# Optimization experiments

Measured on AMD Instinct MI355X. Metric: run time of the kernel, lower is better.

The kernel has to match this reference:

```python
import jax, jax.numpy as jnp
import numpy as np

WS = 8        # window_size
NH = 16       # num_heads
EPS = 1e-5    # BatchNorm eps (inference mode: running_mean=0, running_var=1)

def conv2d(x, w, padding=0, groups=1):
    return jax.lax.conv_general_dilated(
        x, w, (1, 1), [(padding, padding), (padding, padding)],
        dimension_numbers=('NCHW', 'OIHW', 'NCHW'), feature_group_count=groups)

def bn(x, gamma, beta):
    # eval-mode BatchNorm with running_mean=0, running_var=1
    return x * (gamma / jnp.sqrt(1.0 + EPS))[None, :, None, None] + beta[None, :, None, None]

def avgpool(x, kh, kw, ph, pw):
    # torch AvgPool2d with count_include_pad=True: sum over zero-padded window / (kh*kw)
    s = jax.lax.reduce_window(x, 0.0, jax.lax.add, (1, 1, kh, kw), (1, 1, 1, 1),
                              [(0, 0), (0, 0), (ph, ph), (pw, pw)])
    return s / float(kh * kw)

def rel_pos_index(ws):
    coords = np.stack(np.meshgrid(np.arange(ws), np.arange(ws), indexing='ij')).reshape(2, -1)
    rel = (coords[:, :, None] - coords[:, None, :]).transpose(1, 2, 0) + (ws - 1)
    return (rel[..., 0] * (2 * ws - 1) + rel[..., 1]).reshape(-1)

def hge_kernels(W):
    # build 4 directional Sobel kernels + Gaussian-Laplacian from learned scalars
    S0, S45, S90 = W[:, :, 0, 0], W[:, :, 0, 1], W[:, :, 0, 2]
    S135, GL = W[:, :, 1, 0], W[:, :, 2, 2]
    z = jnp.zeros_like(S0)
    k3 = lambda rows: jnp.stack([jnp.stack(r, -1) for r in rows], -2)  # [O,I,3,3]
    w0 = k3([[S0, 2*S0, S0], [z, z, z], [-S0, -2*S0, -S0]])
    w45 = k3([[2*S45, S45, z], [S45, z, -S45], [z, -S45, -2*S45]])
    w90 = k3([[S90, z, -S90], [2*S90, z, -2*S90], [S90, z, -S90]])
    w135 = k3([[z, -S135, -2*S135], [S135, z, -S135], [2*S135, S135, z]])
    a1 = GL * 4.0; a2 = -a1 / 8.0; a3 = -a1 / 16.0
    wGL = jnp.zeros(S0.shape + (5, 5), S0.dtype)
    for i, j, v in [(0,2,a3),(1,1,a3),(1,2,a2),(1,3,a3),(2,0,a3),(2,1,a2),(2,2,a1),
                    (2,3,a2),(2,4,a3),(3,1,a3),(3,2,a2),(3,3,a3),(4,2,a3)]:
        wGL = wGL.at[:, :, i, j].set(v)
    return w0, w45, w90, w135, wGL

def forward(x, ca_h1, ca_w1, ca_fh, ca_fw, l1_w, l1_g, l1_b, l2_w, l2_g, l2_b,
            hge_w, hge_fc_w, hge_fc_b, qkv_w, rel_table, proj_dw, proj_g, proj_b, proj_pw):
    B, C, H, W = x.shape
    d = C // NH
    scale = d ** -0.5
    # --- CA block: coordinate attention (1x1 convs on H- and W-pooled features) ---
    cm = lambda w, t: jnp.einsum('oc,bc...->bo...', w, t)
    s_h = jax.nn.sigmoid(cm(ca_fh, cm(ca_h1, x.mean(3))))   # [B,C,H]
    s_w = jax.nn.sigmoid(cm(ca_fw, cm(ca_w1, x.mean(2))))   # [B,C,W]
    x = x * s_h[:, :, :, None] * s_w[:, :, None, :]
    # --- local branch: 1x1 ConvBN + 3x3 ConvBN + HGE edge operator ---
    local = bn(conv2d(x, l2_w), l2_g, l2_b) + bn(conv2d(x, l1_w, padding=1), l1_g, l1_b)
    w0, w45, w90, w135, wGL = hge_kernels(hge_w)
    feats = jnp.concatenate([conv2d(x, w0, 1), conv2d(x, w45, 1), conv2d(x, w90, 1),
                             conv2d(x, w135, 1), conv2d(x, wGL, 2)], axis=1)  # [B,5C,H,W]
    local = local + conv2d(feats, hge_fc_w) + hge_fc_b[None, :, None, None]
    # --- windowed attention ---
    ph, pw = (-H) % WS, (-W) % WS
    if ph or pw:
        x = jnp.pad(x, ((0, 0), (0, 0), (0, ph), (0, pw)), mode='reflect')
    Hp, Wp = x.shape[2], x.shape[3]
    hh, ww = Hp // WS, Wp // WS
    qkv = conv2d(x, qkv_w)                                   # [B,3C,Hp,Wp]
    qkv = qkv.reshape(B, 3, NH, d, hh, WS, ww, WS)
    qkv = qkv.transpose(1, 0, 4, 6, 2, 5, 7, 3).reshape(3, B * hh * ww, NH, WS * WS, d)
    q, k, v = qkv[0], qkv[1], qkv[2]
    bias = rel_table[rel_pos_index(WS)].reshape(WS * WS, WS * WS, NH).transpose(2, 0, 1)
    dots = jnp.einsum('wnid,wnjd->wnij', q, k) * scale + bias[None]
    attn = jax.nn.softmax(dots, axis=-1)
    o = jnp.einsum('wnij,wnjd->wnid', attn, v)
    o = o.reshape(B, hh, ww, NH, WS, WS, d).transpose(0, 3, 6, 1, 4, 2, 5)
    o = o.reshape(B, C, Hp, Wp)[:, :, :H, :W]
    # --- directional average pooling of attention output ---
    ox = avgpool(jnp.pad(o, ((0, 0), (0, 0), (0, 1), (0, 0)), mode='reflect'), WS, 1, WS // 2 - 1, 0)
    oy = avgpool(jnp.pad(o, ((0, 0), (0, 0), (0, 0), (0, 1)), mode='reflect'), 1, WS, 0, WS // 2 - 1)
    out = ox + oy + local
    # --- pad_out + separable ConvBN projection (depthwise k=ws -> BN -> 1x1) ---
    out = jnp.pad(out, ((0, 0), (0, 0), (0, 1), (0, 1)), mode='reflect')
    out = conv2d(out, proj_dw, padding=(WS - 1) // 2, groups=C)
    out = bn(out, proj_g, proj_b)
    out = conv2d(out, proj_pw)
    return out[:, :, :H, :W]

def setup_inputs() -> dict:
    key = jax.random.key(0)
    ks = jax.random.split(key, 20)
    C = 128
    f32 = jnp.float32
    n = lambda k, sh, s: jax.random.normal(k, sh, f32) * s
    return {
        'x': jax.random.normal(ks[0], (2, C, 256, 256), f32),
        'ca_h1': n(ks[1], (C, C), 0.05), 'ca_w1': n(ks[2], (C, C), 0.05),
        'ca_fh': n(ks[3], (C, C), 0.05), 'ca_fw': n(ks[4], (C, C), 0.05),
        'l1_w': n(ks[5], (C, C, 3, 3), 0.03),
        'l1_g': 1.0 + n(ks[6], (C,), 0.02), 'l1_b': n(ks[7], (C,), 0.02),
        'l2_w': n(ks[8], (C, C, 1, 1), 0.09),
        'l2_g': 1.0 + n(ks[9], (C,), 0.02), 'l2_b': n(ks[10], (C,), 0.02),
        'hge_w': n(ks[11], (C, C, 3, 3), 0.02),
        'hge_fc_w': n(ks[12], (C, 5 * C, 1, 1), 0.02), 'hge_fc_b': n(ks[13], (C,), 0.02),
        'qkv_w': n(ks[14], (3 * C, C, 1, 1), 0.05),
        'rel_table': n(ks[15], ((2 * WS - 1) ** 2, NH), 0.02),
        'proj_dw': n(ks[16], (C, 1, WS, WS), 0.05),
        'proj_g': 1.0 + n(ks[17], (C,), 0.02), 'proj_b': n(ks[18], (C,), 0.02),
        'proj_pw': n(ks[19], (C, C, 1, 1), 0.05),
    }

def reference(x, ca_h1, ca_w1, ca_fh, ca_fw, l1_w, l1_g, l1_b, l2_w, l2_g, l2_b,
              hge_w, hge_fc_w, hge_fc_b, qkv_w, rel_table, proj_dw, proj_g, proj_b, proj_pw):
    return forward(x, ca_h1, ca_w1, ca_fh, ca_fw, l1_w, l1_g, l1_b, l2_w, l2_g, l2_b,
                   hge_w, hge_fc_w, hge_fc_b, qkv_w, rel_table, proj_dw, proj_g, proj_b, proj_pw)
```

## Files before the change

kernel.cpp:

```cpp
#include <hip/hip_runtime.h>

#define BB 2
#define CC 128
#define HWSZ 65536
#define RSQE 0.9999950000374997f
#define ATT_SCALE 0.35355339059327373f

typedef unsigned short u16;
using short8 = __attribute__((ext_vector_type(8))) short;
using f32x4  = __attribute__((ext_vector_type(4))) float;

#if defined(__has_builtin)
# if __has_builtin(__builtin_amdgcn_fdot2_f32_bf16)
#  define HAVE_DOT2 1
# endif
#endif

__device__ __forceinline__ float b2f(u16 u){
  return __uint_as_float(((unsigned int)u) << 16);
}
__device__ __forceinline__ u16 f2b(float f){
  unsigned int v = __float_as_uint(f);
  unsigned int r = (v + 0x7FFFu + ((v >> 16) & 1u)) >> 16;
  return (u16)r;
}

__device__ const int c_DI[13] = {-2,-1,-1,-1, 0, 0,0,0,0, 1,1,1, 2};
__device__ const int c_DJ[13] = { 0,-1, 0, 1,-2,-1,0,1,2,-1,0,1, 0};

__global__ void k_detect(const u16* __restrict__ xr, int* __restrict__ flag){
  __shared__ int ws_[4];
  int tid = threadIdx.x;
  int cnt = 0;
  for (int i = 0; i < 16; ++i){
    u16 u = xr[tid*16 + i];
    int e = (u >> 7) & 0xFF;
    cnt += (e < 100 || e > 141) ? 1 : 0;
  }
  #pragma unroll
  for (int off = 32; off > 0; off >>= 1) cnt += __shfl_down(cnt, off, 64);
  if ((tid & 63) == 0) ws_[tid >> 6] = cnt;
  __syncthreads();
  if (tid == 0) *flag = (ws_[0]+ws_[1]+ws_[2]+ws_[3] > 64) ? 1 : 0;
}

__global__ void k_ingest4(const void* __restrict__ src, u16* __restrict__ dst,
                          int n4, const int* __restrict__ flag){
  int i = blockIdx.x * 256 + threadIdx.x;
  if (i >= n4) return;
  if (*flag){
    float4 f = ((const float4*)src)[i];
    ushort4 r; r.x=f2b(f.x); r.y=f2b(f.y); r.z=f2b(f.z); r.w=f2b(f.w);
    ((ushort4*)dst)[i] = r;
  } else {
    ((ushort4*)dst)[i] = ((const ushort4*)src)[i];
  }
}

struct PtrL { const void* p[19]; };

__global__ void k_ingest_w(PtrL pl, u16* __restrict__ dst, const int* __restrict__ flag){
  const int ends[19] = {16384,32768,49152,65536,212992,213120,213248,229632,229760,
                        229888,377344,459264,459392,508544,512144,520336,520464,520592,536976};
  int g = blockIdx.x * 256 + threadIdx.x;
  int idx = g * 4;
  if (idx >= 536976) return;
  int seg = 0, start = 0;
  #pragma unroll
  for (int s = 0; s < 19; ++s){ if (idx >= ends[s]){ seg = s+1; start = ends[s]; } }
  int local = idx - start;
  const void* sp = pl.p[seg];
  if (*flag){
    float4 f = ((const float4*)sp)[local >> 2];
    ushort4 r; r.x=f2b(f.x); r.y=f2b(f.y); r.z=f2b(f.z); r.w=f2b(f.w);
    *(ushort4*)(dst + idx) = r;
  } else {
    *(ushort4*)(dst + idx) = ((const ushort4*)sp)[local >> 2];
  }
}

__global__ void k_prep_A(const u16* __restrict__ fh, const u16* __restrict__ h1,
                         const u16* __restrict__ fw, const u16* __restrict__ w1,
                         const u16* __restrict__ l1b, const u16* __restrict__ l2b,
                         const u16* __restrict__ fcb,
                         float* __restrict__ A_h, float* __restrict__ A_w,
                         float* __restrict__ biasK){
  int idx = blockIdx.x * 256 + threadIdx.x;
  int o = idx >> 7, c = idx & 127;
  float ah = 0.f, aw = 0.f;
  for (int m = 0; m < 128; ++m){
    ah += b2f(fh[o*128 + m]) * b2f(h1[m*128 + c]);
    aw += b2f(fw[o*128 + m]) * b2f(w1[m*128 + c]);
  }
  A_h[idx] = ah; A_w[idx] = aw;
  if (c == 0) biasK[o] = b2f(l1b[o]) + b2f(l2b[o]) + b2f(fcb[o]);
}

__global__ void k_prep_K(const u16* __restrict__ hge_w, const u16* __restrict__ fc_w,
                         const u16* __restrict__ l1_w, const u16* __restrict__ l1_g,
                         const u16* __restrict__ l2_w, const u16* __restrict__ l2_g,
                         u16* __restrict__ Kwb){
  int idx = blockIdx.x * 256 + threadIdx.x;
  int o = idx >> 7, c = idx & 127;
  float m0=0.f, m45=0.f, m90=0.f, m135=0.f, mgl=0.f;
  const u16* fo = fc_w + o*640;
  for (int m = 0; m < 128; ++m){
    const u16* hw9 = hge_w + (size_t)(m*128 + c)*9;
    m0   += b2f(fo[m      ]) * b2f(hw9[0]);
    m45  += b2f(fo[128 + m]) * b2f(hw9[1]);
    m90  += b2f(fo[256 + m]) * b2f(hw9[2]);
    m135 += b2f(fo[384 + m]) * b2f(hw9[3]);
    mgl  += b2f(fo[512 + m]) * b2f(hw9[8]);
  }
  float g1 = b2f(l1_g[o]) * RSQE;
  float g2 = b2f(l2_g[o]) * RSQE;
  float l1v[9];
  #pragma unroll
  for (int t = 0; t < 9; ++t) l1v[t] = b2f(l1_w[(size_t)idx*9 + t]) * g1;
  float l2v = b2f(l2_w[idx]) * g2;
  float kp[13];
  kp[0]  = -0.25f*mgl;
  kp[1]  =  m0 + 2.f*m45 + m90              - 0.25f*mgl + l1v[0];
  kp[2]  =  2.f*m0 + m45 - m135             - 0.50f*mgl + l1v[1];
  kp[3]  =  m0 - m90 - 2.f*m135             - 0.25f*mgl + l1v[2];
  kp[4]  = -0.25f*mgl;
  kp[5]  =  m45 + 2.f*m90 + m135            - 0.50f*mgl + l1v[3];
  kp[6]  =  4.f*mgl + l1v[4] + l2v;
  kp[7]  = -m45 - 2.f*m90 - m135            - 0.50f*mgl + l1v[5];
  kp[8]  = -0.25f*mgl;
  kp[9]  = -m0 + m90 + 2.f*m135             - 0.25f*mgl + l1v[6];
  kp[10] = -2.f*m0 - m45 + m135             - 0.50f*mgl + l1v[7];
  kp[11] = -m0 - 2.f*m45 - m90              - 0.25f*mgl + l1v[8];
  kp[12] = -0.25f*mgl;
  #pragma unroll
  for (int t = 0; t < 13; ++t) Kwb[t*16384 + idx] = f2b(kp[t]);
}

__global__ void k_means(const u16* __restrict__ x, float* __restrict__ mh, float* __restrict__ mw){
  __shared__ float colpart[4][256];
  int c = blockIdx.x, b = blockIdx.y;
  const u16* xp = x + (size_t)(b*CC + c)*HWSZ;
  int tid = threadIdx.x, lane = tid & 63, wv = tid >> 6;
  float c0=0.f,c1=0.f,c2=0.f,c3=0.f;
  for (int r = 0; r < 64; ++r){
    int h = wv*64 + r;
    ushort4 u = *(const ushort4*)(xp + h*256 + lane*4);
    float v0=b2f(u.x), v1=b2f(u.y), v2=b2f(u.z), v3=b2f(u.w);
    c0+=v0; c1+=v1; c2+=v2; c3+=v3;
    float rs = v0+v1+v2+v3;
    #pragma unroll
    for (int off = 32; off > 0; off >>= 1) rs += __shfl_down(rs, off, 64);
    if (lane == 0) mh[(size_t)(b*CC + c)*256 + h] = rs * (1.0f/256.0f);
  }
  colpart[wv][lane*4+0]=c0; colpart[wv][lane*4+1]=c1;
  colpart[wv][lane*4+2]=c2; colpart[wv][lane*4+3]=c3;
  __syncthreads();
  mw[(size_t)(b*CC + c)*256 + tid] =
    (colpart[0][tid]+colpart[1][tid]+colpart[2][tid]+colpart[3][tid]) * (1.0f/256.0f);
}

__global__ void k_sig(const float* __restrict__ A_h, const float* __restrict__ A_w,
                      const float* __restrict__ mh, const float* __restrict__ mw,
                      float* __restrict__ s_h, float* __restrict__ s_w){
  int o = blockIdx.x, b = blockIdx.y, sel = blockIdx.z, t = threadIdx.x;
  const float* A = sel ? A_w : A_h;
  const float* m = sel ? mw : mh;
  float* s = sel ? s_w : s_h;
  float acc = 0.f;
  for (int c = 0; c < 128; ++c)
    acc += A[o*128 + c] * m[(size_t)(b*CC + c)*256 + t];
  s[(size_t)(b*CC + o)*256 + t] = 1.0f / (1.0f + __expf(-acc));
}

__global__ void k_scale2cl(const u16* __restrict__ cx, const float* __restrict__ s_h,
                           const float* __restrict__ s_w, u16* __restrict__ xcl){
  __shared__ u16 t[16][136];
  int b = blockIdx.z >> 8, h = blockIdx.z & 255;
  int w0 = blockIdx.x * 16;
  int tid = threadIdx.x;
  int ic = tid >> 1, wseg = (tid & 1) * 8;
  uint4 v = *(const uint4*)(cx + (size_t)(b*CC + ic)*HWSZ + h*256 + w0 + wseg);
  float sh = s_h[(size_t)(b*CC + ic)*256 + h];
  const float* swp = s_w + (size_t)(b*CC + ic)*256 + w0 + wseg;
  float4 swa = *(const float4*)swp;
  float4 swb = *(const float4*)(swp + 4);
  u16 tmp[8]; *(uint4*)tmp = v;
  t[wseg+0][ic] = f2b(b2f(tmp[0])*sh*swa.x);
  t[wseg+1][ic] = f2b(b2f(tmp[1])*sh*swa.y);
  t[wseg+2][ic] = f2b(b2f(tmp[2])*sh*swa.z);
  t[wseg+3][ic] = f2b(b2f(tmp[3])*sh*swa.w);
  t[wseg+4][ic] = f2b(b2f(tmp[4])*sh*swb.x);
  t[wseg+5][ic] = f2b(b2f(tmp[5])*sh*swb.y);
  t[wseg+6][ic] = f2b(b2f(tmp[6])*sh*swb.z);
  t[wseg+7][ic] = f2b(b2f(tmp[7])*sh*swb.w);
  __syncthreads();
  int w = tid >> 4, part = (tid & 15) * 8;
  uint4 o = *(const uint4*)&t[w][part];
  *(uint4*)(xcl + ((size_t)(b*256 + h)*256 + (w0 + w))*128 + part) = o;
}

__global__ void k_cf2cl(const u16* __restrict__ src, u16* __restrict__ dst){
  __shared__ u16 t[16][136];
  int b = blockIdx.z >> 8, h = blockIdx.z & 255;
  int w0 = blockIdx.x * 16;
  int tid = threadIdx.x;
  int ic = tid >> 1, wseg = (tid & 1) * 8;
  uint4 v = *(const uint4*)(src + (size_t)(b*CC + ic)*HWSZ + h*256 + w0 + wseg);
  u16 tmp[8]; *(uint4*)tmp = v;
  #pragma unroll
  for (int k = 0; k < 8; ++k) t[wseg + k][ic] = tmp[k];
  __syncthreads();
  int w = tid >> 4, part = (tid & 15) * 8;
  uint4 o = *(const uint4*)&t[w][part];
  *(uint4*)(dst + ((size_t)(b*256 + h)*256 + (w0 + w))*128 + part) = o;
}

__launch_bounds__(256)
__global__ void k_conv5m(const u16* __restrict__ xcl, const u16* __restrict__ Kwb,
                         const float* __restrict__ biasK, u16* __restrict__ outp){
  __shared__ u16 As[128][40];
  __shared__ u16 Bs[128][40];
  int tid = threadIdx.x;
  int wv = tid >> 6, lane = tid & 63;
  int q = lane >> 4, l16 = lane & 15;
  int pt = blockIdx.x;
  int b = pt >> 9, h = (pt >> 1) & 255, w0 = (pt & 1) << 7;
  int mrow = (wv & 1) << 6, nrow = (wv >> 1) << 6;
  int sr = tid >> 2, sp = (tid & 3) << 3;
  const u16* xb_b = xcl + (size_t)b*HWSZ*128;
  f32x4 acc[4][4];
  #pragma unroll
  for (int mt = 0; mt < 4; ++mt)
    #pragma unroll
    for (int nt = 0; nt < 4; ++nt) acc[mt][nt] = (f32x4){0.f,0.f,0.f,0.f};

  for (int kc = 0; kc < 52; ++kc){
    int t = kc >> 2, c0 = (kc & 3) << 5;
    int di = c_DI[t], dj = c_DJ[t];
    int hh2 = h + di;
    bool rowok = (unsigned)hh2 < 256u;
    const u16* rowp = xb_b + (size_t)(rowok ? hh2 : 0)*256*128 + c0 + sp;
    int col0 = w0 + dj + sr;
    int col1 = col0 + 64;
    __syncthreads();
    {
      uint4 va0 = {0,0,0,0}, va1 = {0,0,0,0};
      if (rowok && (unsigned)col0 < 256u) va0 = *(const uint4*)(rowp + col0*128);
      if (rowok && (unsigned)col1 < 256u) va1 = *(const uint4*)(rowp + col1*128);
      *(uint4*)&As[sr][sp] = va0;
      *(uint4*)&As[sr + 64][sp] = va1;
      const u16* Bb = Kwb + t*16384 + c0;
      *(uint4*)&Bs[sr][sp] = *(const uint4*)(Bb + sr*128 + sp);
      *(uint4*)&Bs[sr + 64][sp] = *(const uint4*)(Bb + (sr + 64)*128 + sp);
    }
    __syncthreads();
    short8 af[4], bf[4];
    #pragma unroll
    for (int mt = 0; mt < 4; ++mt) af[mt] = *(const short8*)&As[mrow + mt*16 + l16][q*8];
    #pragma unroll
    for (int nt = 0; nt < 4; ++nt) bf[nt] = *(const short8*)&Bs[nrow + nt*16 + l16][q*8];
    #pragma unroll
    for (int mt = 0; mt < 4; ++mt)
      #pragma unroll
      for (int nt = 0; nt < 4; ++nt)
        acc[mt][nt] = __builtin_amdgcn_mfma_f32_16x16x32_bf16(af[mt], bf[nt], acc[mt][nt], 0, 0, 0);
  }
  #pragma unroll
  for (int nt = 0; nt < 4; ++nt){
    int n = nrow + nt*16 + l16;
    float bv = biasK[n];
    size_t cbase = (size_t)(b*CC + n)*HWSZ + h*256 + w0;
    #pragma unroll
    for (int mt = 0; mt < 4; ++mt){
      int m = mrow + mt*16 + q*4;
      ushort4 st;
      st.x = f2b(acc[mt][nt][0] + bv);
      st.y = f2b(acc[mt][nt][1] + bv);
      st.z = f2b(acc[mt][nt][2] + bv);
      st.w = f2b(acc[mt][nt][3] + bv);
      *(ushort4*)(outp + cbase + m) = st;
    }
  }
}

__launch_bounds__(256)
__global__ void k_mgemm(const u16* __restrict__ Xcl, const u16* __restrict__ W,
                        u16* __restrict__ Y, float* __restrict__ Yf,
                        const int* __restrict__ flag, int nsel, int mode){
  __shared__ u16 As[128][136];
  __shared__ u16 Bs[128][136];
  int tid = threadIdx.x;
  int wv = tid >> 6, lane = tid & 63;
  int q = lane >> 4, l16 = lane & 15;
  int pt = blockIdx.x;
  int b = pt >> 9, h = (pt >> 1) & 255, w0 = (pt & 1) << 7;
  int mrow = (wv & 1) << 6, nrow = (wv >> 1) << 6;
  const u16* Abase = Xcl + ((size_t)(b*256 + h)*256 + w0)*128;
  #pragma unroll
  for (int i = 0; i < 8; ++i){
    int seg = i*256 + tid;
    *(uint4*)&As[seg >> 4][(seg & 15) << 3] = *(const uint4*)(Abase + seg*8);
  }
  for (int sel = 0; sel < nsel; ++sel){
    __syncthreads();
    const u16* Wb = W + sel*16384;
    #pragma unroll
    for (int i = 0; i < 8; ++i){
      int seg = i*256 + tid;
      *(uint4*)&Bs[seg >> 4][(seg & 15) << 3] = *(const uint4*)(Wb + seg*8);
    }
    __syncthreads();
    f32x4 acc[4][4];
    #pragma unroll
    for (int mt = 0; mt < 4; ++mt)
      #pragma unroll
      for (int nt = 0; nt < 4; ++nt) acc[mt][nt] = (f32x4){0.f,0.f,0.f,0.f};
    #pragma unroll
    for (int kc = 0; kc < 4; ++kc){
      short8 af[4], bf[4];
      #pragma unroll
      for (int mt = 0; mt < 4; ++mt) af[mt] = *(const short8*)&As[mrow + mt*16 + l16][kc*32 + q*8];
      #pragma unroll
      for (int nt = 0; nt < 4; ++nt) bf[nt] = *(const short8*)&Bs[nrow + nt*16 + l16][kc*32 + q*8];
      #pragma unroll
      for (int mt = 0; mt < 4; ++mt)
        #pragma unroll
        for (int nt = 0; nt < 4; ++nt)
          acc[mt][nt] = __builtin_amdgcn_mfma_f32_16x16x32_bf16(af[mt], bf[nt], acc[mt][nt], 0, 0, 0);
    }
    if (mode == 0){
      __syncthreads();
      #pragma unroll
      for (int mt = 0; mt < 4; ++mt){
        int m0i = mrow + mt*16 + q*4;
        #pragma unroll
        for (int nt = 0; nt < 4; ++nt){
          int n = nrow + nt*16 + l16;
          Bs[m0i+0][n] = f2b(acc[mt][nt][0]);
          Bs[m0i+1][n] = f2b(acc[mt][nt][1]);
          Bs[m0i+2][n] = f2b(acc[mt][nt][2]);
          Bs[m0i+3][n] = f2b(acc[mt][nt][3]);
        }
      }
      __syncthreads();
      int win = tid >> 4, head = tid & 15;
      size_t obase = (((((size_t)b*32 + (h >> 3))*32 + (w0 >> 3) + win)*3 + sel)*16 + head)*512
                     + (size_t)(h & 7)*64;
      #pragma unroll
      for (int pj = 0; pj < 8; ++pj){
        uint4 vv = *(const uint4*)&Bs[win*8 + pj][head*8];
        *(uint4*)(Y + obase + pj*8) = vv;
      }
    } else {
      int f32o = (Yf != nullptr) && (*flag != 0);
      #pragma unroll
      for (int nt = 0; nt < 4; ++nt){
        int n = nrow + nt*16 + l16;
        size_t cbase = (size_t)(b*CC + n)*HWSZ + h*256 + w0;
        #pragma unroll
        for (int mt = 0; mt < 4; ++mt){
          int m = mrow + mt*16 + q*4;
          if (f32o){
            float4 st; st.x=acc[mt][nt][0]; st.y=acc[mt][nt][1];
            st.z=acc[mt][nt][2]; st.w=acc[mt][nt][3];
            *(float4*)(Yf + cbase + m) = st;
          } else {
            ushort4 st;
            st.x = f2b(acc[mt][nt][0]); st.y = f2b(acc[mt][nt][1]);
            st.z = f2b(acc[mt][nt][2]); st.w = f2b(acc[mt][nt][3]);
            *(ushort4*)(Y + cbase + m) = st;
          }
        }
      }
    }
  }
}

__launch_bounds__(128)
__global__ void k_attn2(const u16* __restrict__ qkvw, const u16* __restrict__ rel,
                        u16* __restrict__ obuf){
  __shared__ float relf[16*228];
  __shared__ u16  qls[2][64][8];
  __shared__ u16  kls[2][64][8];
  __shared__ float vls[2][64][8];
  __shared__ u16  ols[2][64][8];
  int tid = threadIdx.x, wv = tid >> 6, lane = tid & 63;
  int b = blockIdx.z, hh = blockIdx.y, ww0 = blockIdx.x * 2;
  for (int e = tid; e < 3600; e += 128){
    int hd = e / 225, i = e - hd*225;
    relf[hd*228 + i] = b2f(rel[i*16 + hd]);
  }
  int qi = lane >> 3, qj = lane & 7;
  const float* rbase0 = relf + ((qi + 7)*15 + (qj + 7) - 112);
  size_t blkbase = (((size_t)b*32 + hh)*32 + ww0)*3*8192;
  __syncthreads();

  for (int head = 0; head < 16; ++head){
    __syncthreads();
    #pragma unroll
    for (int s = 0; s < 2; ++s){
      int seg = s*128 + tid;
      int sel = seg >> 7, win = (seg >> 6) & 1, pos = seg & 63;
      uint4 v = *(const uint4*)(qkvw + blkbase + (size_t)win*24576 + sel*8192 + head*512 + pos*8);
      if (sel == 0) *(uint4*)&qls[win][pos][0] = v;
      else          *(uint4*)&kls[win][pos][0] = v;
    }
    {
      int win = tid >> 6, pos = tid & 63;
      uint4 raw = *(const uint4*)(qkvw + blkbase + (size_t)win*24576 + 2*8192 + head*512 + pos*8);
      u16 tv[8]; *(uint4*)tv = raw;
      float4 lo, hi;
      lo.x=b2f(tv[0]); lo.y=b2f(tv[1]); lo.z=b2f(tv[2]); lo.w=b2f(tv[3]);
      hi.x=b2f(tv[4]); hi.y=b2f(tv[5]); hi.z=b2f(tv[6]); hi.w=b2f(tv[7]);
      *(float4*)&vls[win][pos][0] = lo;
      *(float4*)&vls[win][pos][4] = hi;
    }
    __syncthreads();

    uint4 qv = *(const uint4*)&qls[wv][lane][0];
    const float* rp = rbase0 + head*228;
    float s[64];
#if HAVE_DOT2
    typedef __bf16 bf2 __attribute__((ext_vector_type(2)));
    bf2 q0 = __builtin_bit_cast(bf2, qv.x), q1 = __builtin_bit_cast(bf2, qv.y);
    bf2 q2 = __builtin_bit_cast(bf2, qv.z), q3 = __builtin_bit_cast(bf2, qv.w);
    #pragma unroll
    for (int kp = 0; kp < 64; ++kp){
      uint4 kv = *(const uint4*)&kls[wv][kp][0];
      float d = __builtin_amdgcn_fdot2_f32_bf16(q3, __builtin_bit_cast(bf2, kv.w), 0.f, false);
      d = __builtin_amdgcn_fdot2_f32_bf16(q2, __builtin_bit_cast(bf2, kv.z), d, false);
      d = __builtin_amdgcn_fdot2_f32_bf16(q1, __builtin_bit_cast(bf2, kv.y), d, false);
      d = __builtin_amdgcn_fdot2_f32_bf16(q0, __builtin_bit_cast(bf2, kv.x), d, false);
      s[kp] = fmaf(d, ATT_SCALE, rp[112 - (kp>>3)*15 - (kp&7)]);
    }
#else
    float qf[8];
    { u16 tq[8]; *(uint4*)tq = qv;
      #pragma unroll
      for (int d = 0; d < 8; ++d) qf[d] = b2f(tq[d]); }
    #pragma unroll
    for (int kp = 0; kp < 64; ++kp){
      uint4 kv = *(const uint4*)&kls[wv][kp][0];
      u16 tk[8]; *(uint4*)tk = kv;
      float d = 0.f;
      #pragma unroll
      for (int dd = 0; dd < 8; ++dd) d = fmaf(qf[dd], b2f(tk[dd]), d);
      s[kp] = fmaf(d, ATT_SCALE, rp[112 - (kp>>3)*15 - (kp&7)]);
    }
#endif
    float t16[16];
    #pragma unroll
    for (int i = 0; i < 16; ++i)
      t16[i] = fmaxf(fmaxf(s[i], s[i+16]), fmaxf(s[i+32], s[i+48]));
    float mx = t16[0];
    #pragma unroll
    for (int i = 1; i < 16; ++i) mx = fmaxf(mx, t16[i]);
    #pragma unroll
    for (int kp = 0; kp < 64; ++kp) s[kp] = __expf(s[kp] - mx);
    #pragma unroll
    for (int i = 0; i < 16; ++i)
      t16[i] = (s[i] + s[i+16]) + (s[i+32] + s[i+48]);
    float sum = t16[0];
    #pragma unroll
    for (int i = 1; i < 16; ++i) sum += t16[i];
    float inv = 1.0f / sum;
    float ov[8] = {0.f,0.f,0.f,0.f,0.f,0.f,0.f,0.f};
    #pragma unroll
    for (int kp = 0; kp < 64; ++kp){
      float4 va = *(const float4*)&vls[wv][kp][0];
      float4 vb = *(const float4*)&vls[wv][kp][4];
      float pp = s[kp];
      ov[0] = fmaf(pp, va.x, ov[0]); ov[1] = fmaf(pp, va.y, ov[1]);
      ov[2] = fmaf(pp, va.z, ov[2]); ov[3] = fmaf(pp, va.w, ov[3]);
      ov[4] = fmaf(pp, vb.x, ov[4]); ov[5] = fmaf(pp, vb.y, ov[5]);
      ov[6] = fmaf(pp, vb.z, ov[6]); ov[7] = fmaf(pp, vb.w, ov[7]);
    }
    u16 po[8];
    #pragma unroll
    for (int d = 0; d < 8; ++d) po[d] = f2b(ov[d] * inv);
    *(uint4*)&ols[wv][lane][0] = *(uint4*)po;
    __syncthreads();
    {
      int win = tid >> 6, d = (tid >> 3) & 7, r = tid & 7;
      u16 pk[8];
      #pragma unroll
      for (int wl = 0; wl < 8; ++wl) pk[wl] = ols[win][r*8 + wl][d];
      *(uint4*)(obuf + (size_t)(b*CC + head*8 + d)*HWSZ + (hh*8 + r)*256 + (ww0 + win)*8)
        = *(uint4*)pk;
    }
  }
}

__launch_bounds__(256)
__global__ void k_pool2(const u16* __restrict__ obuf, u16* __restrict__ localb){
  __shared__ u16 t[71][88];
  int bc = blockIdx.z;
  int h0 = blockIdx.y * 64, w0 = blockIdx.x * 64;
  int tid = threadIdx.x;
  const u16* op = obuf + (size_t)bc * HWSZ;

  for (int e = tid; e < 710; e += 256){
    int tr = e / 10, ci = e - tr*10;
    int gt = h0 - 3 + tr;
    if (gt == 256) gt = 254;
    bool rv = (unsigned)gt <= 255u;
    int g0 = w0 - 8 + ci*8;
    uint4 v = {0,0,0,0};
    if (rv){
      if (g0 >= 0 && g0 <= 248){
        v = *(const uint4*)(op + gt*256 + g0);
      } else {
        u16 tmp[8];
        #pragma unroll
        for (int j = 0; j < 8; ++j){
          int g = g0 + j;
          if (g == 256) g = 254;
          tmp[j] = ((unsigned)g <= 255u) ? op[gt*256 + g] : (u16)0;
        }
        v = *(const uint4*)tmp;
      }
    }
    *(uint4*)&t[tr][ci*8] = v;
  }
  __syncthreads();

  int ty = tid >> 4, tx = tid & 15;
  int r0 = ty*4, c0 = tx*4;
  float sxv[4][4];
  #pragma unroll
  for (int c = 0; c < 4; ++c){
    float col[11];
    #pragma unroll
    for (int i = 0; i < 11; ++i) col[i] = b2f(t[r0+i][c0+8+c]);
    float s = ((col[0]+col[1])+(col[2]+col[3]))+((col[4]+col[5])+(col[6]+col[7]));
    sxv[0][c] = s;
    s += col[8]  - col[0]; sxv[1][c] = s;
    s += col[9]  - col[1]; sxv[2][c] = s;
    s += col[10] - col[2]; sxv[3][c] = s;
  }
  #pragma unroll
  for (int r = 0; r < 4; ++r){
    int rr = r0 + r;
    float pre[11];
    #pragma unroll
    for (int j = 0; j < 11; ++j) pre[j] = b2f(t[rr+3][c0+5+j]);
    float sy0 = ((pre[0]+pre[1])+(pre[2]+pre[3]))+((pre[4]+pre[5])+(pre[6]+pre[7]));
    float sy1 = sy0 + pre[8]  - pre[0];
    float sy2 = sy1 + pre[9]  - pre[1];
    float sy3 = sy2 + pre[10] - pre[2];
    size_t base = (size_t)bc*HWSZ + (size_t)(h0+rr)*256 + (w0+c0);
    ushort4 lv = *(const ushort4*)(localb + base);
    ushort4 st;
    st.x = f2b((sxv[r][0]+sy0)*0.125f + b2f(lv.x));
    st.y = f2b((sxv[r][1]+sy1)*0.125f + b2f(lv.y));
    st.z = f2b((sxv[r][2]+sy2)*0.125f + b2f(lv.z));
    st.w = f2b((sxv[r][3]+sy3)*0.125f + b2f(lv.w));
    *(ushort4*)(localb + base) = st;
  }
}

__launch_bounds__(256)
__global__ void k_dw2(const u16* __restrict__ u_, const u16* __restrict__ dww,
                      const u16* __restrict__ g, const u16* __restrict__ bta,
                      u16* __restrict__ dwout){
  __shared__ u16 xt[71][152];
  int c = blockIdx.z & 127, b = blockIdx.z >> 7;
  int h0 = blockIdx.y * 64, w0 = blockIdx.x * 128;
  int tid = threadIdx.x;
  const u16* up = u_ + (size_t)(b*CC + c)*HWSZ;

  for (int e = tid; e < 71*18; e += 256){
    int tr = e / 18, ci = e - tr*18;
    int gt = h0 - 3 + tr;
    if (gt == 256) gt = 254;
    int g0 = w0 - 8 + ci*8;
    uint4 v = {0,0,0,0};
    if ((unsigned)gt <= 255u){
      if (g0 >= 0 && g0 <= 248){
        v = *(const uint4*)(up + gt*256 + g0);
      } else {
        u16 tmp[8];
        #pragma unroll
        for (int j = 0; j < 8; ++j){
          int gw = g0 + j;
          if (gw == 256) gw = 254;
          tmp[j] = ((unsigned)gw <= 255u) ? up[gt*256 + gw] : (u16)0;
        }
        v = *(const uint4*)tmp;
      }
    }
    *(uint4*)&xt[tr][ci*8] = v;
  }

#if HAVE_DOT2
  typedef __bf16 bf2v __attribute__((ext_vector_type(2)));
  unsigned int wp[32];
  {
    const uint4* wsrc = (const uint4*)(dww + c*64);
    #pragma unroll
    for (int t = 0; t < 8; ++t){
      uint4 v = wsrc[t];
      wp[t*4+0]=v.x; wp[t*4+1]=v.y; wp[t*4+2]=v.z; wp[t*4+3]=v.w;
    }
  }
#else
  float wf[64];
  {
    const u16* wsrc = dww + c*64;
    #pragma unroll
    for (int t = 0; t < 64; ++t) wf[t] = b2f(wsrc[t]);
  }
#endif
  __syncthreads();

  int tx = tid & 15, ty = tid >> 4;
  int r0 = ty*4;
  int cb = tx*8;
  float acc[4][8];
  #pragma unroll
  for (int r = 0; r < 4; ++r)
    #pragma unroll
    for (int k = 0; k < 8; ++k) acc[r][k] = 0.f;

  #pragma unroll
  for (int i = 0; i < 11; ++i){
    const u16* rowp = &xt[r0 + i][cb + 4];
    uint2 av = *(const uint2*)(rowp);
    uint4 mv = *(const uint4*)(rowp + 4);
    uint2 zv = *(const uint2*)(rowp + 12);
    unsigned int d0=av.x, d1=av.y, d2=mv.x, d3=mv.y, d4=mv.z, d5=mv.w, d6=zv.x, d7=zv.y;
    unsigned int dd[8] = {d0,d1,d2,d3,d4,d5,d6,d7};
#if HAVE_DOT2
    unsigned int xp[15];
    #pragma unroll
    for (int t = 1; t < 15; ++t)
      xp[t] = (t & 1) ? ((dd[t>>1] >> 16) | (dd[(t>>1)+1] << 16)) : dd[t>>1];
    #pragma unroll
    for (int dr = 0; dr < 4; ++dr){
      int wr = i - dr;
      if (wr >= 0 && wr < 8){
        #pragma unroll
        for (int k = 0; k < 8; ++k){
          float s = acc[dr][k];
          #pragma unroll
          for (int p = 0; p < 4; ++p)
            s = __builtin_amdgcn_fdot2_f32_bf16(
                  __builtin_bit_cast(bf2v, wp[wr*4+p]),
                  __builtin_bit_cast(bf2v, xp[1+k+2*p]), s, false);
          acc[dr][k] = s;
        }
      }
    }
#else
    float xw[16];
    #pragma unroll
    for (int t = 1; t < 16; ++t){
      unsigned int w32 = dd[t>>1];
      xw[t] = __uint_as_float((t & 1) ? (w32 & 0xFFFF0000u) : (w32 << 16));
    }
    #pragma unroll
    for (int dr = 0; dr < 4; ++dr){
      int wr = i - dr;
      if (wr >= 0 && wr < 8){
        #pragma unroll
        for (int k = 0; k < 8; ++k){
          float s = acc[dr][k];
          #pragma unroll
          for (int j = 0; j < 8; ++j)
            s = fmaf(wf[wr*8+j], xw[1+k+j], s);
          acc[dr][k] = s;
        }
      }
    }
#endif
  }

  float scale = b2f(g[c]) * RSQE;
  float bb = b2f(bta[c]);
  size_t obase = (size_t)(b*CC + c)*HWSZ + (size_t)(h0 + r0)*256 + w0 + cb;
  #pragma unroll
  for (int r = 0; r < 4; ++r){
    u16 po[8];
    #pragma unroll
    for (int k = 0; k < 8; ++k) po[k] = f2b(acc[r][k]*scale + bb);
    *(uint4*)(dwout + obase + (size_t)r*256) = *(uint4*)po;
  }
}

extern "C" void kernel_launch(void* const* d_in, const int* in_sizes, int n_in,
                              void* d_out, int out_size, void* d_ws, size_t ws_size,
                              hipStream_t stream) {
  char* p = (char*)d_ws;
  u16* cx     = (u16*)p; p += 33554432;
  u16* xcl    = (u16*)p; p += 33554432;
  u16* qkvb   = (u16*)p; p += 100663296;
  u16* cw     = (u16*)p; p += 1074176;
  float* A_h    = (float*)p; p += 65536;
  float* A_w    = (float*)p; p += 65536;
  u16*  Kwb     = (u16*)p;  p += 425984;
  float* biasK  = (float*)p; p += 1024;
  float* mh     = (float*)p; p += 262144;
  float* mw     = (float*)p; p += 262144;
  float* s_h    = (float*)p; p += 262144;
  float* s_w    = (float*)p; p += 262144;
  int* flag     = (int*)p;   p += 256;

  u16* localb = (u16*)d_out;
  u16* qkvw   = qkvb;
  u16* obuf   = cx;
  u16* dwbuf  = qkvb;
  u16* dwcl   = xcl;

  const int O_h1=0, O_w1=16384, O_fh=32768, O_fw=49152, O_l1w=65536, O_l1g=212992,
            O_l1b=213120, O_l2w=213248, O_l2g=229632, O_l2b=229760, O_hge=229888,
            O_fcw=377344, O_fcb=459264, O_qkvw=459392, O_rel=508544, O_dw=512144,
            O_pg=520336, O_pb=520464, O_pw=520592;

  k_detect<<<1, 256, 0, stream>>>((const u16*)d_in[0], flag);
  k_ingest4<<<16384, 256, 0, stream>>>(d_in[0], cx, 4194304, flag);
  PtrL pl;
  for (int i = 0; i < 19; ++i) pl.p[i] = d_in[i+1];
  k_ingest_w<<<525, 256, 0, stream>>>(pl, cw, flag);

  k_prep_A<<<64, 256, 0, stream>>>(cw+O_fh, cw+O_h1, cw+O_fw, cw+O_w1,
                                   cw+O_l1b, cw+O_l2b, cw+O_fcb, A_h, A_w, biasK);
  k_prep_K<<<64, 256, 0, stream>>>(cw+O_hge, cw+O_fcw, cw+O_l1w, cw+O_l1g,
                                   cw+O_l2w, cw+O_l2g, Kwb);
  k_means<<<dim3(128, 2), 256, 0, stream>>>(cx, mh, mw);
  k_sig<<<dim3(128, 2, 2), 256, 0, stream>>>(A_h, A_w, mh, mw, s_h, s_w);
  k_scale2cl<<<dim3(16, 1, 512), 256, 0, stream>>>(cx, s_h, s_w, xcl);

  k_conv5m<<<1024, 256, 0, stream>>>(xcl, Kwb, biasK, localb);
  k_mgemm<<<1024, 256, 0, stream>>>(xcl, cw+O_qkvw, qkvw, nullptr, flag, 3, 0);
  k_attn2<<<dim3(16, 32, 2), 128, 0, stream>>>(qkvw, cw+O_rel, obuf);
  k_pool2<<<dim3(4, 4, 256), 256, 0, stream>>>(obuf, localb);
  k_dw2<<<dim3(2, 4, 256), 256, 0, stream>>>(localb, cw+O_dw, cw+O_pg, cw+O_pb, dwbuf);
  k_cf2cl<<<dim3(16, 1, 512), 256, 0, stream>>>(dwbuf, dwcl);
  k_mgemm<<<1024, 256, 0, stream>>>(dwcl, cw+O_pw, (u16*)d_out, (float*)d_out, flag, 1, 1);
}
```

Before: 606.9 us.

## Parallelize window attention across heads with one window per wave

The attention kernel is restructured so each block handles one head for four windows, one window per wave, instead of looping over all 16 heads for two windows. The relative-position table is converted to float once by a new small prep kernel rather than per block. The output is now written directly from registers as scattered 2-byte stores, with no LDS transpose and no per-head syncthreads. This gives far more blocks and fewer barriers, at the cost of less coalesced output writes.

Result: faster. 572.0 us (-5.8%).

```diff
diff --git a/kernel.cpp b/kernel.cpp
--- a/kernel.cpp
+++ b/kernel.cpp
@@ -94,6 +94,13 @@
   }
   A_h[idx] = ah; A_w[idx] = aw;
   if (c == 0) biasK[o] = b2f(l1b[o]) + b2f(l2b[o]) + b2f(fcb[o]);
+}
+
+__global__ void k_prep_rel(const u16* __restrict__ rel, float* __restrict__ relo){
+  int idx = blockIdx.x * 256 + threadIdx.x;
+  if (idx >= 3600) return;
+  int head = idx / 225, i = idx - head*225;
+  relo[idx] = b2f(rel[i*16 + head]);
 }
 
 __global__ void k_prep_K(const u16* __restrict__ hge_w, const u16* __restrict__ fc_w,
@@ -376,119 +383,94 @@
   }
 }
 
-__launch_bounds__(128)
-__global__ void k_attn2(const u16* __restrict__ qkvw, const u16* __restrict__ rel,
+__launch_bounds__(256)
+__global__ void k_attn3(const u16* __restrict__ qkvw, const float* __restrict__ relo,
                         u16* __restrict__ obuf){
-  __shared__ float relf[16*228];
-  __shared__ u16  qls[2][64][8];
-  __shared__ u16  kls[2][64][8];
-  __shared__ float vls[2][64][8];
-  __shared__ u16  ols[2][64][8];
+  __shared__ float relf[228];
+  __shared__ u16  kls[4][64][8];
+  __shared__ float vls[4][64][8];
   int tid = threadIdx.x, wv = tid >> 6, lane = tid & 63;
-  int b = blockIdx.z, hh = blockIdx.y, ww0 = blockIdx.x * 2;
-  for (int e = tid; e < 3600; e += 128){
-    int hd = e / 225, i = e - hd*225;
-    relf[hd*228 + i] = b2f(rel[i*16 + hd]);
-  }
+  int b = blockIdx.z >> 4, head = blockIdx.z & 15;
+  int hh = blockIdx.y, ww = blockIdx.x * 4 + wv;
+
+  for (int e = tid; e < 225; e += 256) relf[e] = relo[head*225 + e];
+
+  size_t base = (((size_t)b*32 + hh)*32 + ww)*3*8192 + (size_t)head*512;
+  uint4 qv = *(const uint4*)(qkvw + base + lane*8);
+  *(uint4*)&kls[wv][lane][0] = *(const uint4*)(qkvw + base + 8192 + lane*8);
+  {
+    uint4 raw = *(const uint4*)(qkvw + base + 16384 + lane*8);
+    u16 tv[8]; *(uint4*)tv = raw;
+    float4 lo, hi;
+    lo.x=b2f(tv[0]); lo.y=b2f(tv[1]); lo.z=b2f(tv[2]); lo.w=b2f(tv[3]);
+    hi.x=b2f(tv[4]); hi.y=b2f(tv[5]); hi.z=b2f(tv[6]); hi.w=b2f(tv[7]);
+    *(float4*)&vls[wv][lane][0] = lo;
+    *(float4*)&vls[wv][lane][4] = hi;
+  }
+  __syncthreads();
+
   int qi = lane >> 3, qj = lane & 7;
-  const float* rbase0 = relf + ((qi + 7)*15 + (qj + 7) - 112);
-  size_t blkbase = (((size_t)b*32 + hh)*32 + ww0)*3*8192;
-  __syncthreads();
-
-  for (int head = 0; head < 16; ++head){
-    __syncthreads();
-    #pragma unroll
-    for (int s = 0; s < 2; ++s){
-      int seg = s*128 + tid;
-      int sel = seg >> 7, win = (seg >> 6) & 1, pos = seg & 63;
-      uint4 v = *(const uint4*)(qkvw + blkbase + (size_t)win*24576 + sel*8192 + head*512 + pos*8);
-      if (sel == 0) *(uint4*)&qls[win][pos][0] = v;
-      else          *(uint4*)&kls[win][pos][0] = v;
-    }
-    {
-      int win = tid >> 6, pos = tid & 63;
-      uint4 raw = *(const uint4*)(qkvw + blkbase + (size_t)win*24576 + 2*8192 + head*512 + pos*8);
-      u16 tv[8]; *(uint4*)tv = raw;
-      float4 lo, hi;
-      lo.x=b2f(tv[0]); lo.y=b2f(tv[1]); lo.z=b2f(tv[2]); lo.w=b2f(tv[3]);
-      hi.x=b2f(tv[4]); hi.y=b2f(tv[5]); hi.z=b2f(tv[6]); hi.w=b2f(tv[7]);
-      *(float4*)&vls[win][pos][0] = lo;
-      *(float4*)&vls[win][pos][4] = hi;
-    }
-    __syncthreads();
-
-    uint4 qv = *(const uint4*)&qls[wv][lane][0];
-    const float* rp = rbase0 + head*228;
-    float s[64];
+  const float* rbase = relf + (qi + 7)*15 + (qj + 7);
+  float s[64];
 #if HAVE_DOT2
-    typedef __bf16 bf2 __attribute__((ext_vector_type(2)));
-    bf2 q0 = __builtin_bit_cast(bf2, qv.x), q1 = __builtin_bit_cast(bf2, qv.y);
-    bf2 q2 = __builtin_bit_cast(bf2, qv.z), q3 = __builtin_bit_cast(bf2, qv.w);
-    #pragma unroll
-    for (int kp = 0; kp < 64; ++kp){
-      uint4 kv = *(const uint4*)&kls[wv][kp][0];
-      float d = __builtin_amdgcn_fdot2_f32_bf16(q3, __builtin_bit_cast(bf2, kv.w), 0.f, false);
-      d = __builtin_amdgcn_fdot2_f32_bf16(q2, __builtin_bit_cast(bf2, kv.z), d, false);
-      d = __builtin_amdgcn_fdot2_f32_bf16(q1, __builtin_bit_cast(bf2, kv.y), d, false);
-      d = __builtin_amdgcn_fdot2_f32_bf16(q0, __builtin_bit_cast(bf2, kv.x), d, false);
-      s[kp] = fmaf(d, ATT_SCALE, rp[112 - (kp>>3)*15 - (kp&7)]);
-    }
+  typedef __bf16 bf2 __attribute__((ext_vector_type(2)));
+  bf2 q0 = __builtin_bit_cast(bf2, qv.x), q1 = __builtin_bit_cast(bf2, qv.y);
+  bf2 q2 = __builtin_bit_cast(bf2, qv.z), q3 = __builtin_bit_cast(bf2, qv.w);
+  #pragma unroll
+  for (int kp = 0; kp < 64; ++kp){
+    uint4 kv = *(const uint4*)&kls[wv][kp][0];
+    float d = __builtin_amdgcn_fdot2_f32_bf16(q3, __builtin_bit_cast(bf2, kv.w), 0.f, false);
+    d = __builtin_amdgcn_fdot2_f32_bf16(q2, __builtin_bit_cast(bf2, kv.z), d, false);
+    d = __builtin_amdgcn_fdot2_f32_bf16(q1, __builtin_bit_cast(bf2, kv.y), d, false);
+    d = __builtin_amdgcn_fdot2_f32_bf16(q0, __builtin_bit_cast(bf2, kv.x), d, false);
+    s[kp] = fmaf(d, ATT_SCALE, rbase[-((kp>>3)*15 + (kp&7))]);
+  }
 #else
-    float qf[8];
-    { u16 tq[8]; *(uint4*)tq = qv;
-      #pragma unroll
-      for (int d = 0; d < 8; ++d) qf[d] = b2f(tq[d]); }
-    #pragma unroll
-    for (int kp = 0; kp < 64; ++kp){
-      uint4 kv = *(const uint4*)&kls[wv][kp][0];
-      u16 tk[8]; *(uint4*)tk = kv;
-      float d = 0.f;
-      #pragma unroll
-      for (int dd = 0; dd < 8; ++dd) d = fmaf(qf[dd], b2f(tk[dd]), d);
-      s[kp] = fmaf(d, ATT_SCALE, rp[112 - (kp>>3)*15 - (kp&7)]);
-    }
+  float qf[8];
+  { u16 tq[8]; *(uint4*)tq = qv;
+    #pragma unroll
+    for (int d = 0; d < 8; ++d) qf[d] = b2f(tq[d]); }
+  #pragma unroll
+  for (int kp = 0; kp < 64; ++kp){
+    uint4 kv = *(const uint4*)&kls[wv][kp][0];
+    u16 tk[8]; *(uint4*)tk = kv;
+    float d = 0.f;
+    #pragma unroll
+    for (int dd = 0; dd < 8; ++dd) d = fmaf(qf[dd], b2f(tk[dd]), d);
+    s[kp] = fmaf(d, ATT_SCALE, rbase[-((kp>>3)*15 + (kp&7))]);
+  }
 #endif
-    float t16[16];
-    #pragma unroll
-    for (int i = 0; i < 16; ++i)
-      t16[i] = fmaxf(fmaxf(s[i], s[i+16]), fmaxf(s[i+32], s[i+48]));
-    float mx = t16[0];
-    #pragma unroll
-    for (int i = 1; i < 16; ++i) mx = fmaxf(mx, t16[i]);
-    #pragma unroll
-    for (int kp = 0; kp < 64; ++kp) s[kp] = __expf(s[kp] - mx);
-    #pragma unroll
-    for (int i = 0; i < 16; ++i)
-      t16[i] = (s[i] + s[i+16]) + (s[i+32] + s[i+48]);
-    float sum = t16[0];
-    #pragma unroll
-    for (int i = 1; i < 16; ++i) sum += t16[i];
-    float inv = 1.0f / sum;
-    float ov[8] = {0.f,0.f,0.f,0.f,0.f,0.f,0.f,0.f};
-    #pragma unroll
-    for (int kp = 0; kp < 64; ++kp){
-      float4 va = *(const float4*)&vls[wv][kp][0];
-      float4 vb = *(const float4*)&vls[wv][kp][4];
-      float pp = s[kp];
-      ov[0] = fmaf(pp, va.x, ov[0]); ov[1] = fmaf(pp, va.y, ov[1]);
-      ov[2] = fmaf(pp, va.z, ov[2]); ov[3] = fmaf(pp, va.w, ov[3]);
-      ov[4] = fmaf(pp, vb.x, ov[4]); ov[5] = fmaf(pp, vb.y, ov[5]);
-      ov[6] = fmaf(pp, vb.z, ov[6]); ov[7] = fmaf(pp, vb.w, ov[7]);
-    }
-    u16 po[8];
-    #pragma unroll
-    for (int d = 0; d < 8; ++d) po[d] = f2b(ov[d] * inv);
-    *(uint4*)&ols[wv][lane][0] = *(uint4*)po;
-    __syncthreads();
-    {
-      int win = tid >> 6, d = (tid >> 3) & 7, r = tid & 7;
-      u16 pk[8];
-      #pragma unroll
-      for (int wl = 0; wl < 8; ++wl) pk[wl] = ols[win][r*8 + wl][d];
-      *(uint4*)(obuf + (size_t)(b*CC + head*8 + d)*HWSZ + (hh*8 + r)*256 + (ww0 + win)*8)
-        = *(uint4*)pk;
-    }
-  }
+  float t16[16];
+  #pragma unroll
+  for (int i = 0; i < 16; ++i)
+    t16[i] = fmaxf(fmaxf(s[i], s[i+16]), fmaxf(s[i+32], s[i+48]));
+  float mx = t16[0];
+  #pragma unroll
+  for (int i = 1; i < 16; ++i) mx = fmaxf(mx, t16[i]);
+  #pragma unroll
+  for (int kp = 0; kp < 64; ++kp) s[kp] = __expf(s[kp] - mx);
+  #pragma unroll
+  for (int i = 0; i < 16; ++i)
+    t16[i] = (s[i] + s[i+16]) + (s[i+32] + s[i+48]);
+  float sum = t16[0];
+  #pragma unroll
+  for (int i = 1; i < 16; ++i) sum += t16[i];
+  float inv = 1.0f / sum;
+  float ov[8] = {0.f,0.f,0.f,0.f,0.f,0.f,0.f,0.f};
+  #pragma unroll
+  for (int kp = 0; kp < 64; ++kp){
+    float4 va = *(const float4*)&vls[wv][kp][0];
+    float4 vb = *(const float4*)&vls[wv][kp][4];
+    float pp = s[kp];
+    ov[0] = fmaf(pp, va.x, ov[0]); ov[1] = fmaf(pp, va.y, ov[1]);
+    ov[2] = fmaf(pp, va.z, ov[2]); ov[3] = fmaf(pp, va.w, ov[3]);
+    ov[4] = fmaf(pp, vb.x, ov[4]); ov[5] = fmaf(pp, vb.y, ov[5]);
+    ov[6] = fmaf(pp, vb.z, ov[6]); ov[7] = fmaf(pp, vb.w, ov[7]);
+  }
+  size_t obase = (size_t)(b*CC + head*8)*HWSZ + (size_t)(hh*8 + qi)*256 + ww*8 + qj;
+  #pragma unroll
+  for (int d = 0; d < 8; ++d)
+    obuf[obase + (size_t)d*HWSZ] = f2b(ov[d] * inv);
 }
 
 __launch_bounds__(256)
@@ -704,6 +686,7 @@
   float* s_h    = (float*)p; p += 262144;
   float* s_w    = (float*)p; p += 262144;
   int* flag     = (int*)p;   p += 256;
+  float* relo   = (float*)p; p += 16384;
 
   u16* localb = (u16*)d_out;
   u16* qkvw   = qkvb;
@@ -724,6 +707,7 @@
 
   k_prep_A<<<64, 256, 0, stream>>>(cw+O_fh, cw+O_h1, cw+O_fw, cw+O_w1,
                                    cw+O_l1b, cw+O_l2b, cw+O_fcb, A_h, A_w, biasK);
+  k_prep_rel<<<15, 256, 0, stream>>>(cw+O_rel, relo);
   k_prep_K<<<64, 256, 0, stream>>>(cw+O_hge, cw+O_fcw, cw+O_l1w, cw+O_l1g,
                                    cw+O_l2w, cw+O_l2g, Kwb);
   k_means<<<dim3(128, 2), 256, 0, stream>>>(cx, mh, mw);
@@ -732,7 +716,7 @@
 
   k_conv5m<<<1024, 256, 0, stream>>>(xcl, Kwb, biasK, localb);
   k_mgemm<<<1024, 256, 0, stream>>>(xcl, cw+O_qkvw, qkvw, nullptr, flag, 3, 0);
-  k_attn2<<<dim3(16, 32, 2), 128, 0, stream>>>(qkvw, cw+O_rel, obuf);
+  k_attn3<<<dim3(8, 32, 32), 256, 0, stream>>>(qkvw, relo, obuf);
   k_pool2<<<dim3(4, 4, 256), 256, 0, stream>>>(obuf, localb);
   k_dw2<<<dim3(2, 4, 256), 256, 0, stream>>>(localb, cw+O_dw, cw+O_pg, cw+O_pb, dwbuf);
   k_cf2cl<<<dim3(16, 1, 512), 256, 0, stream>>>(dwbuf, dwcl);
```
